# Kernel tuning notes

Hardware: AMD Instinct MI355X
Metric: run time of the kernel (lower is better)

The kernel has to match this reference:

```python
import jax, jax.numpy as jnp
from jax import lax
import numpy as np

W_SSIM = 0.5
W_SMOOTH = 0.1
W_LR = 1.0
C1 = 0.01 ** 2
C2 = 0.03 ** 2


def avg3(x):
    # 3x3 stride-1 VALID average pool (matches F.avg_pool2d(x, 3, 1))
    return lax.reduce_window(x, 0.0, lax.add, (1, 1, 3, 3), (1, 1, 1, 1), 'VALID') / 9.0


def resize_ac(img, oh, ow):
    # bilinear resize with align_corners=True, separable gathers
    B, C, H, W = img.shape
    ys = jnp.linspace(0.0, H - 1.0, oh)
    xs = jnp.linspace(0.0, W - 1.0, ow)
    y0 = jnp.floor(ys).astype(jnp.int32); y1 = jnp.minimum(y0 + 1, H - 1); wy = ys - y0
    x0 = jnp.floor(xs).astype(jnp.int32); x1 = jnp.minimum(x0 + 1, W - 1); wx = xs - x0
    r = img[:, :, y0, :] * (1.0 - wy)[None, None, :, None] + img[:, :, y1, :] * wy[None, None, :, None]
    return r[:, :, :, x0] * (1.0 - wx) + r[:, :, :, x1] * wx


def warp_h(img, disp, sign):
    # horizontal bilinear warp: sample img at x + sign*disp (disp in units of image width),
    # align_corners=True pixel mapping, zeros padding outside the image.
    B, C, H, W = img.shape
    xb = jnp.linspace(0.0, 1.0, W)
    px = (xb[None, None, :] + sign * disp[:, 0, :, :]) * (W - 1)  # [B,H,W] pixel coords
    x0 = jnp.floor(px); f = px - x0
    x0i = x0.astype(jnp.int32); x1i = x0i + 1
    v0 = ((x0i >= 0) & (x0i < W)).astype(img.dtype)
    v1 = ((x1i >= 0) & (x1i < W)).astype(img.dtype)
    i0 = jnp.broadcast_to(jnp.clip(x0i, 0, W - 1)[:, None], (B, C, H, W))
    i1 = jnp.broadcast_to(jnp.clip(x1i, 0, W - 1)[:, None], (B, C, H, W))
    g0 = jnp.take_along_axis(img, i0, axis=3)
    g1 = jnp.take_along_axis(img, i1, axis=3)
    return g0 * (v0 * (1.0 - f))[:, None] + g1 * (v1 * f)[:, None]


def ssim(x, y):
    mu_x = avg3(x); mu_y = avg3(y)
    sig_x = avg3(x * x) - mu_x ** 2
    sig_y = avg3(y * y) - mu_y ** 2
    sig_xy = avg3(x * y) - mu_x * mu_y
    s = ((2 * mu_x * mu_y + C1) * (2 * sig_xy + C2)) / ((mu_x ** 2 + mu_y ** 2 + C1) * (sig_x + sig_y + C2))
    return jnp.clip((1.0 - s) / 2.0, 0.0, 1.0)


def smoothness(disp, img):
    dgx = disp[:, :, :, :-1] - disp[:, :, :, 1:]
    dgy = disp[:, :, :-1, :] - disp[:, :, 1:, :]
    igx = img[:, :, :, :-1] - img[:, :, :, 1:]
    igy = img[:, :, :-1, :] - img[:, :, 1:, :]
    wx = jnp.exp(-jnp.mean(jnp.abs(igx), axis=1, keepdims=True))
    wy = jnp.exp(-jnp.mean(jnp.abs(igy), axis=1, keepdims=True))
    return jnp.mean(jnp.abs(dgx * wx)) + jnp.mean(jnp.abs(dgy * wy))


def compute_loss(disps, left, right):
    B, _, H, W = left.shape
    img_loss = 0.0
    lr_loss = 0.0
    sm_loss = 0.0
    for i, d in enumerate(disps):
        r = 2 ** i
        h, w = H // r, W // r
        lpy = left if i == 0 else resize_ac(left, h, w)
        rpy = right if i == 0 else resize_ac(right, h, w)
        dl = d[:, 0:1]; dr = d[:, 1:2]
        left_est = warp_h(rpy, dl, -1.0)
        right_est = warp_h(lpy, dr, 1.0)
        rl_disp = warp_h(dr, dl, -1.0)
        lr_disp = warp_h(dl, dr, 1.0)
        l1_l = jnp.mean(jnp.abs(left_est - lpy))
        l1_r = jnp.mean(jnp.abs(right_est - rpy))
        ss_l = jnp.mean(ssim(left_est, lpy))
        ss_r = jnp.mean(ssim(right_est, rpy))
        img_loss = img_loss + W_SSIM * ss_l + (1 - W_SSIM) * l1_l + W_SSIM * ss_r + (1 - W_SSIM) * l1_r
        lr_loss = lr_loss + jnp.mean(jnp.abs(rl_disp - dl)) + jnp.mean(jnp.abs(lr_disp - dr))
        sm_loss = sm_loss + (smoothness(dl, lpy) + smoothness(dr, rpy)) / r
    return img_loss + W_SMOOTH * sm_loss + W_LR * lr_loss


def setup_inputs() -> dict:
    key = jax.random.key(0)
    ks = jax.random.split(key, 6)
    B, H, W = 16, 384, 768
    inp = {}
    for i in range(4):
        r = 2 ** i
        # disparities in units of image width; scaled to realistic ~[0, 0.1]
        inp[f'disp{i}'] = jax.random.uniform(ks[i], (B, 2, H // r, W // r), dtype=jnp.float32) * 0.1
    inp['left_image'] = jax.random.uniform(ks[4], (B, 3, H, W), dtype=jnp.float32)
    inp['right_image'] = jax.random.uniform(ks[5], (B, 3, H, W), dtype=jnp.float32)
    return inp


def reference(disp0, disp1, disp2, disp3, left_image, right_image):
    return compute_loss([disp0, disp1, disp2, disp3], left_image, right_image)
```

## Files before the change

kernel.cpp:

```cpp
#include <hip/hip_runtime.h>
#include <math.h>

#define C1F 1.0e-4f
#define C2F 9.0e-4f
#define TX 32
#define TY 8
#define NSTAGE ((TY + 2) * (TX + 2))


struct F3 { float x, y, z; };
__device__ __forceinline__ F3 ld3(const float* p) { return *(const F3*)p; }

struct ScaleArgs {
    const float* disp;
    const float* lp;
    const float* rp;
    int h, w, nx, ny, blk0, accoff, ntiles;
};

__device__ __forceinline__ float2 f2(float v) { return make_float2(v, v); }
__device__ __forceinline__ float2 f2abs(float2 a) {
    return make_float2(fabsf(a.x), fabsf(a.y));
}

__device__ __forceinline__ void warp_coeffs(float px, int W, int& i0, int& i1,
                                            float& w0, float& w1) {
    float x0f = floorf(px);
    float f = px - x0f;
    int x0i = (int)x0f;
    int x1i = x0i + 1;
    float v0 = (x0i >= 0 && x0i < W) ? 1.f : 0.f;
    float v1 = (x1i >= 0 && x1i < W) ? 1.f : 0.f;
    i0 = min(max(x0i, 0), W - 1);
    i1 = min(max(x1i, 0), W - 1);
    w0 = v0 * (1.f - f);
    w1 = v1 * f;
}

template<int N>
__device__ __forceinline__ void block_acc(const float* vals, float* gacc) {
    __shared__ float sacc[N];
    if (threadIdx.x < N) sacc[threadIdx.x] = 0.f;
    __syncthreads();
#pragma unroll
    for (int k = 0; k < N; ++k) {
        float v = vals[k];
#pragma unroll
        for (int off = 32; off > 0; off >>= 1) v += __shfl_down(v, off, 64);
        if ((threadIdx.x & 63) == 0) atomicAdd(&sacc[k], v);
    }
    __syncthreads();
    if (threadIdx.x < N) atomicAdd(&gacc[threadIdx.x], sacc[threadIdx.x]);
}

__device__ __forceinline__ int xcd_swz(int orig, int n) {
    int q = n >> 3, r = n & 7;
    int x = orig & 7;
    int base = (x < r) ? x * (q + 1) : r * (q + 1) + (x - r) * q;
    return base + (orig >> 3);
}

template<bool PACKED>
__device__ void fused_tile(const ScaleArgs& sa, int t,
                           float* __restrict__ accbase,
                           float4* __restrict__ simg,
                           float2* __restrict__ sdisp) {
    const int h = sa.h, w = sa.w;
    float* acc = accbase + sa.accoff;

    const int tileX = t % sa.nx;
    int t2 = t / sa.nx;
    const int tileY = t2 % sa.ny;
    const int b = t2 / sa.ny;

    const int xo0 = tileX * TX, yo0 = tileY * TY;
    const int tid = threadIdx.x;
    const float Wm1 = (float)(w - 1);
    const float invWm1 = 1.f / Wm1;
    const int chs = h * w;

    const float* __restrict__ dl_base = sa.disp + (b * 2 + 0) * chs;
    const float* __restrict__ dr_base = sa.disp + (b * 2 + 1) * chs;

    if (PACKED) {
        const float* __restrict__ Lb = sa.lp + (size_t)b * chs * 3;
        const float* __restrict__ Rb = sa.rp + (size_t)b * chs * 3;
        for (int i = tid; i < NSTAGE; i += 256) {
            int sx = i % (TX + 2);
            int sy = i / (TX + 2);
            int x = min(max(xo0 - 1 + sx, 0), w - 1);
            int y = min(max(yo0 - 1 + sy, 0), h - 1);
            int off = y * w + x;
            float dl = dl_base[off];
            float dr = dr_base[off];
            float xb = (float)x * invWm1;
            int i0L, i1L, i0R, i1R;
            float w0L, w1L, w0R, w1R;
            warp_coeffs((xb - dl) * Wm1, w, i0L, i1L, w0L, w1L);
            warp_coeffs((xb + dr) * Wm1, w, i0R, i1R, w0R, w1R);
            const float* rowL = Lb + (size_t)(y * w) * 3;
            const float* rowR = Rb + (size_t)(y * w) * 3;
            F3 lv = ld3(rowL + 3 * x);
            F3 gl0 = ld3(rowL + 3 * i0R);
            F3 gl1 = ld3(rowL + 3 * i1R);
            F3 rv = ld3(rowR + 3 * x);
            F3 gr0 = ld3(rowR + 3 * i0L);
            F3 gr1 = ld3(rowR + 3 * i1L);
            sdisp[i] = make_float2(dl, dr);
            simg[0 * NSTAGE + i] = make_float4(gr0.x * w0L + gr1.x * w1L,
                                               gl0.x * w0R + gl1.x * w1R, lv.x, rv.x);
            simg[1 * NSTAGE + i] = make_float4(gr0.y * w0L + gr1.y * w1L,
                                               gl0.y * w0R + gl1.y * w1R, lv.y, rv.y);
            simg[2 * NSTAGE + i] = make_float4(gr0.z * w0L + gr1.z * w1L,
                                               gl0.z * w0R + gl1.z * w1R, lv.z, rv.z);
        }
    } else {
        const float* __restrict__ limg = sa.lp + (size_t)b * 3 * chs;
        const float* __restrict__ rimg = sa.rp + (size_t)b * 3 * chs;
        for (int i = tid; i < NSTAGE; i += 256) {
            int sx = i % (TX + 2);
            int sy = i / (TX + 2);
            int x = min(max(xo0 - 1 + sx, 0), w - 1);
            int y = min(max(yo0 - 1 + sy, 0), h - 1);
            int off = y * w + x;
            float dl = dl_base[off];
            float dr = dr_base[off];
            float xb = (float)x * invWm1;
            int i0L, i1L, i0R, i1R;
            float w0L, w1L, w0R, w1R;
            warp_coeffs((xb - dl) * Wm1, w, i0L, i1L, w0L, w1L);
            warp_coeffs((xb + dr) * Wm1, w, i0R, i1R, w0R, w1R);
            int rowoff = y * w;
            sdisp[i] = make_float2(dl, dr);
#pragma unroll
            for (int c = 0; c < 3; ++c) {
                int co = c * chs + rowoff;
                float le = rimg[co + i0L] * w0L + rimg[co + i1L] * w1L;
                float re = limg[co + i0R] * w0R + limg[co + i1R] * w1R;
                simg[c * NSTAGE + i] = make_float4(le, re, limg[co + x], rimg[co + x]);
            }
        }
    }
    __syncthreads();

    float sums[8] = {0.f, 0.f, 0.f, 0.f, 0.f, 0.f, 0.f, 0.f};
    const int tx = tid % TX, ty = tid / TX;
    const int x = xo0 + tx, y = yo0 + ty;
    if (x < w && y < h) {
        const int s = (ty + 1) * (TX + 2) + (tx + 1);
        float2 dd = sdisp[s];
        float dl = dd.x, dr = dd.y;
#pragma unroll
        for (int c = 0; c < 3; ++c) {
            float4 v = simg[c * NSTAGE + s];
            float2 d = f2abs(make_float2(v.x, v.y) - make_float2(v.z, v.w));
            sums[0] += d.x;
            sums[1] += d.y;
        }
        {
            float xb = (float)x * invWm1;
            int i0, i1; float w0, w1;
            warp_coeffs((xb - dl) * Wm1, w, i0, i1, w0, w1);
            const float* dr_row = dr_base + y * w;
            float rl = dr_row[i0] * w0 + dr_row[i1] * w1;
            sums[2] += fabsf(rl - dl);
            warp_coeffs((xb + dr) * Wm1, w, i0, i1, w0, w1);
            const float* dl_row = dl_base + y * w;
            float lr = dl_row[i0] * w0 + dl_row[i1] * w1;
            sums[3] += fabsf(lr - dr);
        }
        const float third = 1.f / 3.f;
        if (x < w - 1) {
            float2 d1 = sdisp[s + 1];
            float2 alr = f2(0.f);
#pragma unroll
            for (int c = 0; c < 3; ++c) {
                float4 v = simg[c * NSTAGE + s];
                float4 v1 = simg[c * NSTAGE + s + 1];
                alr = alr + f2abs(make_float2(v.z, v.w) - make_float2(v1.z, v1.w));
            }
            sums[4] += fabsf((dl - d1.x) * __expf(-alr.x * third)) +
                       fabsf((dr - d1.y) * __expf(-alr.y * third));
        }
        if (y < h - 1) {
            float2 d1 = sdisp[s + (TX + 2)];
            float2 alr = f2(0.f);
#pragma unroll
            for (int c = 0; c < 3; ++c) {
                float4 v = simg[c * NSTAGE + s];
                float4 v1 = simg[c * NSTAGE + s + (TX + 2)];
                alr = alr + f2abs(make_float2(v.z, v.w) - make_float2(v1.z, v1.w));
            }
            sums[5] += fabsf((dl - d1.x) * __expf(-alr.x * third)) +
                       fabsf((dr - d1.y) * __expf(-alr.y * third));
        }
        if (x >= 1 && x <= w - 2 && y >= 1 && y <= h - 2) {
            const float2 inv9 = f2(1.f / 9.f);
            const float2 c1 = f2(C1F), c2 = f2(C2F);
            const float2 two = f2(2.f), one = f2(1.f), half_ = f2(0.5f);
#pragma unroll 1
            for (int c = 0; c < 3; ++c) {
                float2 sX = f2(0.f), sY = f2(0.f);
                float2 sXX = f2(0.f), sYY = f2(0.f), sXY = f2(0.f);
#pragma unroll
                for (int dy = 0; dy < 3; ++dy) {
#pragma unroll
                    for (int dx = 0; dx < 3; ++dx) {
                        float4 v = simg[c * NSTAGE + (ty + dy) * (TX + 2) + (tx + dx)];
                        float2 a = make_float2(v.x, v.y);
                        float2 bb = make_float2(v.z, v.w);
                        sX = sX + a;
                        sY = sY + bb;
                        sXX = sXX + a * a;
                        sYY = sYY + bb * bb;
                        sXY = sXY + a * bb;
                    }
                }
                float2 mx = sX * inv9, my = sY * inv9;
                float2 vx = sXX * inv9 - mx * mx;
                float2 vy = sYY * inv9 - my * my;
                float2 vxy = sXY * inv9 - mx * my;
                float2 num = (two * mx * my + c1) * (two * vxy + c2);
                float2 den = (mx * mx + my * my + c1) * (vx + vy + c2);
                float2 ss = make_float2(num.x * __builtin_amdgcn_rcpf(den.x),
                                        num.y * __builtin_amdgcn_rcpf(den.y));
                float2 v = (one - ss) * half_;
                sums[6] += fminf(fmaxf(v.x, 0.f), 1.f);
                sums[7] += fminf(fmaxf(v.y, 0.f), 1.f);
            }
        }
    }
    block_acc<8>(sums, acc);
}

template<bool PACKED>
__global__ void __launch_bounds__(256, 4)
k_tiles(ScaleArgs s0, ScaleArgs s1, ScaleArgs s2, ScaleArgs s3,
        float* __restrict__ accbase) {
    __shared__ float4 simg[3 * NSTAGE];
    __shared__ float2 sdisp[NSTAGE];

    int blk = (int)blockIdx.x;
    ScaleArgs sa = (blk >= s3.blk0) ? s3
                 : (blk >= s2.blk0) ? s2
                 : (blk >= s1.blk0) ? s1 : s0;
    int t = xcd_swz(blk - sa.blk0, sa.ntiles);
    fused_tile<PACKED>(sa, t, accbase, simg, sdisp);
}

__global__ void k_final(const float* __restrict__ acc, float* __restrict__ out) {
    if (threadIdx.x != 0 || blockIdx.x != 0) return;
    float img = 0.f, lr = 0.f, sm = 0.f;
    for (int i = 0; i < 4; ++i) {
        int r = 1 << i;
        int h = 384 >> i, w = 768 >> i;
        const float* a = acc + i * 8;
        float Nl1 = 16.f * 3.f * (float)h * (float)w;
        float Nss = 16.f * 3.f * (float)(h - 2) * (float)(w - 2);
        float Nlr = 16.f * (float)h * (float)w;
        float Nsx = 16.f * (float)h * (float)(w - 1);
        float Nsy = 16.f * (float)(h - 1) * (float)w;
        img += 0.5f * (a[6] / Nss) + 0.5f * (a[0] / Nl1)
             + 0.5f * (a[7] / Nss) + 0.5f * (a[1] / Nl1);
        lr += a[2] / Nlr + a[3] / Nlr;
        sm += (a[4] / Nsx + a[5] / Nsy) / (float)r;
    }
    out[0] = img + 0.1f * sm + 1.0f * lr;
}

#define HW 294912
#define HALF_PX 4718592
#define RPK_BLOCKS 36864
#define N1P 2359296
#define N2P 589824
#define N3P 147456
#define RESB 12096
#define N1E 7077888LL
#define N2E 1769472LL
#define N3E 442368LL
#define PL_BLOCKS 36288

template<int OH, int OW>
__device__ __forceinline__ void resize_pos(int idx,
                                           const float* __restrict__ left,
                                           const float* __restrict__ right,
                                           float* __restrict__ lo,
                                           float* __restrict__ ro) {
    const int half = 16 * OH * OW;
    const float* src = left;
    float* dst = lo;
    if (idx >= half) { src = right; dst = ro; idx -= half; }
    int x = idx % OW;
    int t = idx / OW;
    int y = t % OH;
    int b = t / OH;
    float sy = (float)(384 - 1) / (float)(OH - 1);
    float sx = (float)(768 - 1) / (float)(OW - 1);
    float fy = y * sy;
    float fx = x * sx;
    int y0 = (int)floorf(fy); float wy = fy - (float)y0;
    int x0 = (int)floorf(fx); float wx = fx - (float)x0;
    int y1 = min(y0 + 1, 383); y0 = min(y0, 383);
    int x1 = min(x0 + 1, 767); x0 = min(x0, 767);
    F3 o;
    float* po = &o.x;
#pragma unroll
    for (int c = 0; c < 3; ++c) {
        const float* p = src + (size_t)(b * 3 + c) * HW;
        float a00 = p[y0 * 768 + x0];
        float a10 = p[y1 * 768 + x0];
        float a01 = p[y0 * 768 + x1];
        float a11 = p[y1 * 768 + x1];
        float r0 = a00 * (1.f - wy) + a10 * wy;
        float r1 = a01 * (1.f - wy) + a11 * wy;
        po[c] = r0 * (1.f - wx) + r1 * wx;
    }
    *(F3*)(dst + (size_t)idx * 3) = o;
}

template<int OH, int OW>
__device__ __forceinline__ void resize_elem(long long idx,
                                            const float* __restrict__ left,
                                            const float* __restrict__ right,
                                            float* __restrict__ lo,
                                            float* __restrict__ ro) {
    const long long half = (long long)16 * 3 * OH * OW;
    const float* src = left;
    float* dst = lo;
    if (idx >= half) { src = right; dst = ro; idx -= half; }
    int x = (int)(idx % OW);
    long long t = idx / OW;
    int y = (int)(t % OH);
    t /= OH;
    int c = (int)(t % 3);
    int b = (int)(t / 3);
    float sy = (float)(384 - 1) / (float)(OH - 1);
    float sx = (float)(768 - 1) / (float)(OW - 1);
    float fy = y * sy;
    float fx = x * sx;
    int y0 = (int)floorf(fy); float wy = fy - (float)y0;
    int x0 = (int)floorf(fx); float wx = fx - (float)x0;
    int y1 = min(y0 + 1, 383); y0 = min(y0, 383);
    int x1 = min(x0 + 1, 767); x0 = min(x0, 767);
    const float* p = src + (size_t)(b * 3 + c) * HW;
    float a00 = p[y0 * 768 + x0];
    float a10 = p[y1 * 768 + x0];
    float a01 = p[y0 * 768 + x1];
    float a11 = p[y1 * 768 + x1];
    float r0 = a00 * (1.f - wy) + a10 * wy;
    float r1 = a01 * (1.f - wy) + a11 * wy;
    dst[(((size_t)b * 3 + c) * OH + y) * OW + x] = r0 * (1.f - wx) + r1 * wx;
}

__global__ void __launch_bounds__(256)
k_prelude_pk(const float* __restrict__ left, const float* __restrict__ right,
             float* __restrict__ acc,
             float* __restrict__ pkL, float* __restrict__ pkR,
             float* __restrict__ p1L, float* __restrict__ p1R,
             float* __restrict__ p2L, float* __restrict__ p2R,
             float* __restrict__ p3L, float* __restrict__ p3R) {
    int blk = (int)blockIdx.x, tid = threadIdx.x;
    if (blk == 0 && tid < 128) acc[tid] = 0.f;
    if (blk < RPK_BLOCKS) {
        int idx = blk * 256 + tid;
        const float* src = left;
        float* dst = pkL;
        if (idx >= HALF_PX) { src = right; dst = pkR; idx -= HALF_PX; }
        int b = idx / HW;
        int rem = idx - b * HW;
        const float* p = src + (size_t)b * 3 * HW + rem;
        F3 v;
        v.x = p[0]; v.y = p[HW]; v.z = p[2 * HW];
        *(F3*)(dst + (size_t)idx * 3) = v;
        return;
    }
    int idx = (blk - RPK_BLOCKS) * 256 + tid;
    if (idx < N1P)              resize_pos<192, 384>(idx, left, right, p1L, p1R);
    else if (idx < N1P + N2P)   resize_pos<96, 192>(idx - N1P, left, right, p2L, p2R);
    else                        resize_pos<48, 96>(idx - N1P - N2P, left, right, p3L, p3R);
}

__global__ void __launch_bounds__(256)
k_prelude_pl(const float* __restrict__ left, const float* __restrict__ right,
             float* __restrict__ acc,
             float* __restrict__ lo1, float* __restrict__ ro1,
             float* __restrict__ lo2, float* __restrict__ ro2,
             float* __restrict__ lo3, float* __restrict__ ro3) {
    int blk = (int)blockIdx.x, tid = threadIdx.x;
    if (blk == 0 && tid < 128) acc[tid] = 0.f;
    long long idx = (long long)blk * 256 + tid;
    if (idx < N1E)                  resize_elem<192, 384>(idx, left, right, lo1, ro1);
    else if (idx < N1E + N2E)       resize_elem<96, 192>(idx - N1E, left, right, lo2, ro2);
    else                            resize_elem<48, 96>(idx - N1E - N2E, left, right, lo3, ro3);
}

extern "C" void kernel_launch(void* const* d_in, const int* in_sizes, int n_in,
                              void* d_out, int out_size, void* d_ws, size_t ws_size,
                              hipStream_t stream) {
    const int B = 16, H = 384, W = 768;
    const float* disp[4] = {(const float*)d_in[0], (const float*)d_in[1],
                            (const float*)d_in[2], (const float*)d_in[3]};
    const float* left = (const float*)d_in[4];
    const float* right = (const float*)d_in[5];
    float* out = (float*)d_out;
    float* acc = (float*)d_ws;

    const size_t szF = (size_t)B * H * W * 3;
    const size_t sz1p = (size_t)B * 192 * 384 * 3;
    const size_t sz2p = (size_t)B * 96 * 192 * 3;
    const size_t sz3p = (size_t)B * 48 * 96 * 3;
    const size_t need_pk = (256 + 2 * (szF + sz1p + sz2p + sz3p)) * sizeof(float);
    const bool packed = ws_size >= need_pk;

    ScaleArgs sa[4];
    int blk0 = 0;
    for (int i = 0; i < 4; ++i) {
        int r = 1 << i;
        int h = H / r, w = W / r;
        sa[i].disp = disp[i];
        sa[i].h = h;
        sa[i].w = w;
        sa[i].nx = w / TX;
        sa[i].ny = h / TY;
        sa[i].accoff = i * 8;
        sa[i].ntiles = sa[i].nx * sa[i].ny * B;
        sa[i].blk0 = blk0;
        blk0 += sa[i].ntiles;
    }
    int nTotal = blk0;

    if (packed) {
        float* pkL = acc + 256;
        float* pkR = pkL + szF;
        float* p1L = pkR + szF;
        float* p1R = p1L + sz1p;
        float* p2L = p1R + sz1p;
        float* p2R = p2L + sz2p;
        float* p3L = p2R + sz2p;
        float* p3R = p3L + sz3p;
        const float* lp[4] = {pkL, p1L, p2L, p3L};
        const float* rp[4] = {pkR, p1R, p2R, p3R};
        for (int i = 0; i < 4; ++i) { sa[i].lp = lp[i]; sa[i].rp = rp[i]; }

        hipLaunchKernelGGL(k_prelude_pk, dim3(RPK_BLOCKS + RESB), dim3(256), 0, stream,
                           left, right, acc, pkL, pkR, p1L, p1R, p2L, p2R, p3L, p3R);
        hipLaunchKernelGGL(k_tiles<true>, dim3((unsigned)nTotal), dim3(256), 0, stream,
                           sa[0], sa[1], sa[2], sa[3], acc);
    } else {
        float* pyr = acc + 256;
        size_t sz1 = (size_t)B * 3 * 192 * 384;
        size_t sz2 = (size_t)B * 3 * 96 * 192;
        size_t sz3 = (size_t)B * 3 * 48 * 96;
        float* lp1 = pyr;
        float* rp1 = lp1 + sz1;
        float* lp2 = rp1 + sz1;
        float* rp2 = lp2 + sz2;
        float* lp3 = rp2 + sz2;
        float* rp3 = lp3 + sz3;
        const float* lp[4] = {left, lp1, lp2, lp3};
        const float* rp[4] = {right, rp1, rp2, rp3};
        for (int i = 0; i < 4; ++i) { sa[i].lp = lp[i]; sa[i].rp = rp[i]; }

        hipLaunchKernelGGL(k_prelude_pl, dim3(PL_BLOCKS), dim3(256), 0, stream,
                           left, right, acc, lp1, rp1, lp2, rp2, lp3, rp3);
        hipLaunchKernelGGL(k_tiles<false>, dim3((unsigned)nTotal), dim3(256), 0, stream,
                           sa[0], sa[1], sa[2], sa[3], acc);
    }
    hipLaunchKernelGGL(k_final, dim3(1), dim3(64), 0, stream, acc, out);
}
```

Before: 520.5 us.

## Batch tile staging loads, raise occupancy bound, vectorize channel packing

```diff
diff --git a/kernel.cpp b/kernel.cpp
--- a/kernel.cpp
+++ b/kernel.cpp
@@ -85,34 +85,56 @@
     if (PACKED) {
         const float* __restrict__ Lb = sa.lp + (size_t)b * chs * 3;
         const float* __restrict__ Rb = sa.rp + (size_t)b * chs * 3;
-        for (int i = tid; i < NSTAGE; i += 256) {
-            int sx = i % (TX + 2);
-            int sy = i / (TX + 2);
-            int x = min(max(xo0 - 1 + sx, 0), w - 1);
-            int y = min(max(yo0 - 1 + sy, 0), h - 1);
-            int off = y * w + x;
-            float dl = dl_base[off];
-            float dr = dr_base[off];
-            float xb = (float)x * invWm1;
-            int i0L, i1L, i0R, i1R;
-            float w0L, w1L, w0R, w1R;
-            warp_coeffs((xb - dl) * Wm1, w, i0L, i1L, w0L, w1L);
-            warp_coeffs((xb + dr) * Wm1, w, i0R, i1R, w0R, w1R);
-            const float* rowL = Lb + (size_t)(y * w) * 3;
-            const float* rowR = Rb + (size_t)(y * w) * 3;
-            F3 lv = ld3(rowL + 3 * x);
-            F3 gl0 = ld3(rowL + 3 * i0R);
-            F3 gl1 = ld3(rowL + 3 * i1R);
-            F3 rv = ld3(rowR + 3 * x);
-            F3 gr0 = ld3(rowR + 3 * i0L);
-            F3 gr1 = ld3(rowR + 3 * i1L);
-            sdisp[i] = make_float2(dl, dr);
-            simg[0 * NSTAGE + i] = make_float4(gr0.x * w0L + gr1.x * w1L,
-                                               gl0.x * w0R + gl1.x * w1R, lv.x, rv.x);
-            simg[1 * NSTAGE + i] = make_float4(gr0.y * w0L + gr1.y * w1L,
-                                               gl0.y * w0R + gl1.y * w1R, lv.y, rv.y);
-            simg[2 * NSTAGE + i] = make_float4(gr0.z * w0L + gr1.z * w1L,
-                                               gl0.z * w0R + gl1.z * w1R, lv.z, rv.z);
+        const int nk = (tid + 256 < NSTAGE) ? 2 : 1;
+        int xs[2], offr[2];
+        float dlv[2], drv[2];
+#pragma unroll
+        for (int k = 0; k < 2; ++k) {
+            if (k < nk) {
+                int i = tid + (k << 8);
+                int sx = i % (TX + 2);
+                int sy = i / (TX + 2);
+                int x = min(max(xo0 - 1 + sx, 0), w - 1);
+                int y = min(max(yo0 - 1 + sy, 0), h - 1);
+                xs[k] = x; offr[k] = y * w;
+                dlv[k] = dl_base[offr[k] + x];
+                drv[k] = dr_base[offr[k] + x];
+            }
+        }
+        F3 lv[2], rv[2], g0[2], g1[2], h0[2], h1[2];
+        float w0L[2], w1L[2], w0R[2], w1R[2];
+#pragma unroll
+        for (int k = 0; k < 2; ++k) {
+            if (k < nk) {
+                float xb = (float)xs[k] * invWm1;
+                int i0L, i1L, i0R, i1R;
+                warp_coeffs((xb - dlv[k]) * Wm1, w, i0L, i1L, w0L[k], w1L[k]);
+                warp_coeffs((xb + drv[k]) * Wm1, w, i0R, i1R, w0R[k], w1R[k]);
+                const float* rowL = Lb + (size_t)offr[k] * 3;
+                const float* rowR = Rb + (size_t)offr[k] * 3;
+                lv[k] = ld3(rowL + 3 * xs[k]);
+                rv[k] = ld3(rowR + 3 * xs[k]);
+                g0[k] = ld3(rowR + 3 * i0L);
+                g1[k] = ld3(rowR + 3 * i1L);
+                h0[k] = ld3(rowL + 3 * i0R);
+                h1[k] = ld3(rowL + 3 * i1R);
+            }
+        }
+#pragma unroll
+        for (int k = 0; k < 2; ++k) {
+            if (k < nk) {
+                int i = tid + (k << 8);
+                sdisp[i] = make_float2(dlv[k], drv[k]);
+                simg[0 * NSTAGE + i] = make_float4(g0[k].x * w0L[k] + g1[k].x * w1L[k],
+                                                   h0[k].x * w0R[k] + h1[k].x * w1R[k],
+                                                   lv[k].x, rv[k].x);
+                simg[1 * NSTAGE + i] = make_float4(g0[k].y * w0L[k] + g1[k].y * w1L[k],
+                                                   h0[k].y * w0R[k] + h1[k].y * w1R[k],
+                                                   lv[k].y, rv[k].y);
+                simg[2 * NSTAGE + i] = make_float4(g0[k].z * w0L[k] + g1[k].z * w1L[k],
+                                                   h0[k].z * w0R[k] + h1[k].z * w1R[k],
+                                                   lv[k].z, rv[k].z);
+            }
         }
     } else {
         const float* __restrict__ limg = sa.lp + (size_t)b * 3 * chs;
@@ -234,7 +256,7 @@
 }
 
 template<bool PACKED>
-__global__ void __launch_bounds__(256, 4)
+__global__ void __launch_bounds__(256, 6)
 k_tiles(ScaleArgs s0, ScaleArgs s1, ScaleArgs s2, ScaleArgs s3,
         float* __restrict__ accbase) {
     __shared__ float4 simg[3 * NSTAGE];
@@ -269,8 +291,9 @@
 }
 
 #define HW 294912
-#define HALF_PX 4718592
-#define RPK_BLOCKS 36864
+#define HW4 73728
+#define HALF_P4 1179648
+#define RPK4_BLOCKS 9216
 #define N1P 2359296
 #define N2P 589824
 #define N3P 147456
@@ -361,20 +384,24 @@
              float* __restrict__ p3L, float* __restrict__ p3R) {
     int blk = (int)blockIdx.x, tid = threadIdx.x;
     if (blk == 0 && tid < 128) acc[tid] = 0.f;
-    if (blk < RPK_BLOCKS) {
+    if (blk < RPK4_BLOCKS) {
         int idx = blk * 256 + tid;
         const float* src = left;
         float* dst = pkL;
-        if (idx >= HALF_PX) { src = right; dst = pkR; idx -= HALF_PX; }
-        int b = idx / HW;
-        int rem = idx - b * HW;
-        const float* p = src + (size_t)b * 3 * HW + rem;
-        F3 v;
-        v.x = p[0]; v.y = p[HW]; v.z = p[2 * HW];
-        *(F3*)(dst + (size_t)idx * 3) = v;
+        if (idx >= HALF_P4) { src = right; dst = pkR; idx -= HALF_P4; }
+        int b = idx / HW4;
+        int rem = idx - b * HW4;
+        const float4* pr = (const float4*)(src + (size_t)b * 3 * HW);
+        float4 r = pr[rem];
+        float4 g = pr[HW4 + rem];
+        float4 bb = pr[2 * HW4 + rem];
+        float4* od = (float4*)(dst + (size_t)b * HW * 3) + (size_t)rem * 3;
+        od[0] = make_float4(r.x, g.x, bb.x, r.y);
+        od[1] = make_float4(g.y, bb.y, r.z, g.z);
+        od[2] = make_float4(bb.z, r.w, g.w, bb.w);
         return;
     }
-    int idx = (blk - RPK_BLOCKS) * 256 + tid;
+    int idx = (blk - RPK4_BLOCKS) * 256 + tid;
     if (idx < N1P)              resize_pos<192, 384>(idx, left, right, p1L, p1R);
     else if (idx < N1P + N2P)   resize_pos<96, 192>(idx - N1P, left, right, p2L, p2R);
     else                        resize_pos<48, 96>(idx - N1P - N2P, left, right, p3L, p3R);
@@ -442,7 +469,7 @@
         const float* rp[4] = {pkR, p1R, p2R, p3R};
         for (int i = 0; i < 4; ++i) { sa[i].lp = lp[i]; sa[i].rp = rp[i]; }
 
-        hipLaunchKernelGGL(k_prelude_pk, dim3(RPK_BLOCKS + RESB), dim3(256), 0, stream,
+        hipLaunchKernelGGL(k_prelude_pk, dim3(RPK4_BLOCKS + RESB), dim3(256), 0, stream,
                            left, right, acc, pkL, pkR, p1L, p1R, p2L, p2R, p3L, p3R);
         hipLaunchKernelGGL(k_tiles<true>, dim3((unsigned)nTotal), dim3(256), 0, stream,
                            sa[0], sa[1], sa[2], sa[3], acc);
```

Result: no change. 522.9 us (+0.5%).
